# Optimization experiments

Hardware: AMD Instinct MI355X
Metric: run time of the kernel (lower is better)

## Reference

```python
import jax, jax.numpy as jnp
import numpy as np

NTOKEN, NINP, NCLASS = 50000, 256, 16
B, L = 32, 2048
INITRANGE = 0.1


def setup_inputs() -> dict:
    key = jax.random.key(0)
    k1, k2, k3 = jax.random.split(key, 3)
    inp = jax.random.randint(k1, (B, L), 0, NTOKEN).astype(jnp.int64) if jax.config.jax_enable_x64 else jax.random.randint(k1, (B, L), 0, NTOKEN)
    mask = jnp.ones((B, L), dtype=jnp.float32)
    enc_w = jax.random.uniform(k2, (NTOKEN + 1, NINP), jnp.float32, -INITRANGE, INITRANGE)
    dec_w = jax.random.uniform(k3, (NCLASS, NINP), jnp.float32, -INITRANGE, INITRANGE)
    return {"input": inp, "mask": mask, "enc_w": enc_w, "dec_w": dec_w}


def reference(input, mask, enc_w, dec_w):
    # emb: [B, L, D], masked embedding gather
    emb = enc_w[input] * mask[:, :, None]
    # scores_l = emb_l . sum_k emb_k  ==  (emb @ emb^T).sum(axis=2)
    emb_sum = emb.sum(axis=1)                         # [B, D]
    scores = jnp.einsum('bld,bd->bl', emb, emb_sum)   # [B, L]
    y = jnp.exp(scores) * mask                        # faithful: no max-subtract
    attn = y / y.sum(axis=1, keepdims=True)           # [B, L]
    output = jnp.einsum('bld,bl->bd', emb, attn)      # weighted-sum pooling
    # residual mean pooling
    lens = mask.sum(axis=1, keepdims=True)            # [B, 1]
    avg = emb_sum / lens
    out = output + avg
    return out @ dec_w.T                              # [B, NCLASS]
```

## Files before the change

kernel.cpp:

```cpp
#include <hip/hip_runtime.h>
#include <math.h>

#define BB 32
#define LL 2048
#define DD 256
#define NC 16
#define SPLIT 32
#define TPB 256
#define TOK_PER_CHUNK (LL / SPLIT)
#define TOK_PER_WAVE  (TOK_PER_CHUNK / 4)
#define PF 8


__global__ __launch_bounds__(TPB) void kA_partial(
    const int* __restrict__ idx, const float* __restrict__ mask,
    const float4* __restrict__ enc4,
    float* __restrict__ pes, float* __restrict__ plen) {
  const int b     = blockIdx.x / SPLIT;
  const int chunk = blockIdx.x % SPLIT;
  const int wave  = threadIdx.x >> 6;
  const int lane  = threadIdx.x & 63;
  const int tid   = threadIdx.x;
  const int l0 = chunk * TOK_PER_CHUNK + wave * TOK_PER_WAVE;

  int   id_r[TOK_PER_WAVE];
  float m_r[TOK_PER_WAVE];
  #pragma unroll
  for (int t = 0; t < TOK_PER_WAVE; ++t) {
    id_r[t] = idx[b * LL + l0 + t];
    m_r[t]  = mask[b * LL + l0 + t];
  }

  float4 acc = {0.f, 0.f, 0.f, 0.f};
  float lenacc = 0.f;
  #pragma unroll
  for (int g = 0; g < TOK_PER_WAVE; g += PF) {
    float4 v[PF];
    #pragma unroll
    for (int t = 0; t < PF; ++t)
      v[t] = enc4[(size_t)id_r[g + t] * (DD / 4) + lane];
    #pragma unroll
    for (int t = 0; t < PF; ++t) {
      const float m = m_r[g + t];
      acc.x += v[t].x * m; acc.y += v[t].y * m;
      acc.z += v[t].z * m; acc.w += v[t].w * m;
      lenacc += m;
    }
  }

  __shared__ float lds[4][DD];
  __shared__ float llds[4];
  lds[wave][lane * 4 + 0] = acc.x;
  lds[wave][lane * 4 + 1] = acc.y;
  lds[wave][lane * 4 + 2] = acc.z;
  lds[wave][lane * 4 + 3] = acc.w;
  if (lane == 0) llds[wave] = lenacc;
  __syncthreads();

  const float s = lds[0][tid] + lds[1][tid] + lds[2][tid] + lds[3][tid];
  pes[(chunk * BB + b) * DD + tid] = s;
  if (tid == 0) plen[chunk * BB + b] = llds[0] + llds[1] + llds[2] + llds[3];
}

__global__ __launch_bounds__(TPB) void kR1(
    const float* __restrict__ pes, const float* __restrict__ plen,
    float* __restrict__ emb_sum, float* __restrict__ lens) {
  const int b = blockIdx.x;
  const int tid = threadIdx.x;
  float s = 0.f;
  #pragma unroll
  for (int c = 0; c < SPLIT; ++c) s += pes[(c * BB + b) * DD + tid];
  emb_sum[b * DD + tid] = s;
  if (tid < 64) {
    float v = (tid < SPLIT) ? plen[tid * BB + b] : 0.f;
    #pragma unroll
    for (int off = 16; off > 0; off >>= 1) v += __shfl_xor(v, off);
    if (tid == 0) lens[b] = v;
  }
}

__global__ __launch_bounds__(TPB) void kB_partial(
    const int* __restrict__ idx, const float* __restrict__ mask,
    const float4* __restrict__ enc4, const float* __restrict__ emb_sum,
    float* __restrict__ pout, float* __restrict__ pys) {
  const int b     = blockIdx.x / SPLIT;
  const int chunk = blockIdx.x % SPLIT;
  const int wave  = threadIdx.x >> 6;
  const int lane  = threadIdx.x & 63;
  const int tid   = threadIdx.x;
  const int l0 = chunk * TOK_PER_CHUNK + wave * TOK_PER_WAVE;

  const float4 es = reinterpret_cast<const float4*>(emb_sum)[b * (DD / 4) + lane];

  int   id_r[TOK_PER_WAVE];
  float m_r[TOK_PER_WAVE];
  #pragma unroll
  for (int t = 0; t < TOK_PER_WAVE; ++t) {
    id_r[t] = idx[b * LL + l0 + t];
    m_r[t]  = mask[b * LL + l0 + t];
  }

  float4 acc = {0.f, 0.f, 0.f, 0.f};
  float ys = 0.f;
  #pragma unroll
  for (int g = 0; g < TOK_PER_WAVE; g += PF) {
    float4 v[PF];
    #pragma unroll
    for (int t = 0; t < PF; ++t)
      v[t] = enc4[(size_t)id_r[g + t] * (DD / 4) + lane];
    #pragma unroll
    for (int t = 0; t < PF; ++t) {
      const float m = m_r[g + t];
      float d = v[t].x * es.x + v[t].y * es.y + v[t].z * es.z + v[t].w * es.w;
      #pragma unroll
      for (int off = 32; off > 0; off >>= 1) d += __shfl_xor(d, off);
      const float score = d * m;
      const float y = expf(score) * m;
      const float ym = y * m;
      acc.x += ym * v[t].x; acc.y += ym * v[t].y;
      acc.z += ym * v[t].z; acc.w += ym * v[t].w;
      ys += y;
    }
  }

  __shared__ float lds[4][DD];
  __shared__ float ylds[4];
  lds[wave][lane * 4 + 0] = acc.x;
  lds[wave][lane * 4 + 1] = acc.y;
  lds[wave][lane * 4 + 2] = acc.z;
  lds[wave][lane * 4 + 3] = acc.w;
  if (lane == 0) ylds[wave] = ys;
  __syncthreads();

  const float s = lds[0][tid] + lds[1][tid] + lds[2][tid] + lds[3][tid];
  pout[(chunk * BB + b) * DD + tid] = s;
  if (tid == 0) pys[chunk * BB + b] = ylds[0] + ylds[1] + ylds[2] + ylds[3];
}

__global__ __launch_bounds__(TPB) void kR2head(
    const float* __restrict__ pout, const float* __restrict__ pys,
    const float* __restrict__ emb_sum, const float* __restrict__ lens,
    const float* __restrict__ dec_w, float* __restrict__ out) {
  const int b = blockIdx.x;
  const int tid = threadIdx.x;
  const int wave = tid >> 6;
  const int lane = tid & 63;

  float os = 0.f;
  #pragma unroll
  for (int c = 0; c < SPLIT; ++c) os += pout[(c * BB + b) * DD + tid];

  __shared__ float ysum_s;
  __shared__ float vec[DD];
  if (tid < 64) {
    float v = (tid < SPLIT) ? pys[tid * BB + b] : 0.f;
    #pragma unroll
    for (int off = 16; off > 0; off >>= 1) v += __shfl_xor(v, off);
    if (tid == 0) ysum_s = v;
  }
  __syncthreads();

  vec[tid] = os / ysum_s + emb_sum[b * DD + tid] / lens[b];
  __syncthreads();

  const float4 vv = *reinterpret_cast<const float4*>(&vec[lane * 4]);
  #pragma unroll
  for (int cc = 0; cc < 4; ++cc) {
    const int c = wave * 4 + cc;
    const float4 dw = reinterpret_cast<const float4*>(dec_w)[c * (DD / 4) + lane];
    float d = vv.x * dw.x + vv.y * dw.y + vv.z * dw.z + vv.w * dw.w;
    #pragma unroll
    for (int off = 32; off > 0; off >>= 1) d += __shfl_xor(d, off);
    if (lane == 0) out[b * NC + c] = d;
  }
}

extern "C" void kernel_launch(void* const* d_in, const int* in_sizes, int n_in,
                              void* d_out, int out_size, void* d_ws, size_t ws_size,
                              hipStream_t stream) {
  const int*   idx   = (const int*)d_in[0];
  const float* mask  = (const float*)d_in[1];
  const float* enc_w = (const float*)d_in[2];
  const float* dec_w = (const float*)d_in[3];
  float* out = (float*)d_out;

  float* ws = (float*)d_ws;
  float* pes     = ws;
  float* plen    = pes + SPLIT * BB * DD;
  float* pout    = plen + SPLIT * BB;
  float* pys     = pout + SPLIT * BB * DD;
  float* emb_sum = pys + SPLIT * BB;
  float* lens    = emb_sum + BB * DD;

  const dim3 block(TPB);
  const dim3 gridP(BB * SPLIT);
  hipLaunchKernelGGL(kA_partial, gridP, block, 0, stream,
                     idx, mask, (const float4*)enc_w, pes, plen);
  hipLaunchKernelGGL(kR1, dim3(BB), block, 0, stream, pes, plen, emb_sum, lens);
  hipLaunchKernelGGL(kB_partial, gridP, block, 0, stream,
                     idx, mask, (const float4*)enc_w, emb_sum, pout, pys);
  hipLaunchKernelGGL(kR2head, dim3(BB), block, 0, stream,
                     pout, pys, emb_sum, lens, dec_w, out);
}
```

Before: 33.12 us.

## Fuse first reduction into second pass and rebalance split counts

Removes the separate kR1 reduction kernel. Each block of the second pass now reduces the per-chunk partial embedding sums itself into shared memory, and chunk 0 writes emb_sum and lens. The second pass split drops from 32 to 16 chunks, giving more tokens per wave, and the first pass now issues all 16 gathers up front instead of in groups of 8. This saves one kernel launch and its dependency gap, but every block of the second pass re-reads the 32 partials, and the deeper register arrays can raise register pressure.

```diff
diff --git a/kernel.cpp b/kernel.cpp
--- a/kernel.cpp
+++ b/kernel.cpp
@@ -5,47 +5,49 @@
 #define LL 2048
 #define DD 256
 #define NC 16
-#define SPLIT 32
 #define TPB 256
-#define TOK_PER_CHUNK (LL / SPLIT)
-#define TOK_PER_WAVE  (TOK_PER_CHUNK / 4)
-#define PF 8
+
+#define SA 32
+#define TA_CHUNK (LL / SA)
+#define TA_WAVE  (TA_CHUNK / 4)
+
+#define SB 16
+#define TB_CHUNK (LL / SB)
+#define TB_WAVE  (TB_CHUNK / 4)
+#define PFB 8
 
 
 __global__ __launch_bounds__(TPB) void kA_partial(
     const int* __restrict__ idx, const float* __restrict__ mask,
     const float4* __restrict__ enc4,
     float* __restrict__ pes, float* __restrict__ plen) {
-  const int b     = blockIdx.x / SPLIT;
-  const int chunk = blockIdx.x % SPLIT;
+  const int b     = blockIdx.x / SA;
+  const int chunk = blockIdx.x % SA;
   const int wave  = threadIdx.x >> 6;
   const int lane  = threadIdx.x & 63;
   const int tid   = threadIdx.x;
-  const int l0 = chunk * TOK_PER_CHUNK + wave * TOK_PER_WAVE;
-
-  int   id_r[TOK_PER_WAVE];
-  float m_r[TOK_PER_WAVE];
-  #pragma unroll
-  for (int t = 0; t < TOK_PER_WAVE; ++t) {
+  const int l0 = chunk * TA_CHUNK + wave * TA_WAVE;
+
+  int   id_r[TA_WAVE];
+  float m_r[TA_WAVE];
+  #pragma unroll
+  for (int t = 0; t < TA_WAVE; ++t) {
     id_r[t] = idx[b * LL + l0 + t];
     m_r[t]  = mask[b * LL + l0 + t];
   }
+  float4 v_r[TA_WAVE];
+  #pragma unroll
+  for (int t = 0; t < TA_WAVE; ++t)
+    v_r[t] = enc4[(size_t)id_r[t] * (DD / 4) + lane];
 
   float4 acc = {0.f, 0.f, 0.f, 0.f};
   float lenacc = 0.f;
   #pragma unroll
-  for (int g = 0; g < TOK_PER_WAVE; g += PF) {
-    float4 v[PF];
-    #pragma unroll
-    for (int t = 0; t < PF; ++t)
-      v[t] = enc4[(size_t)id_r[g + t] * (DD / 4) + lane];
-    #pragma unroll
-    for (int t = 0; t < PF; ++t) {
-      const float m = m_r[g + t];
-      acc.x += v[t].x * m; acc.y += v[t].y * m;
-      acc.z += v[t].z * m; acc.w += v[t].w * m;
-      lenacc += m;
-    }
+  for (int t = 0; t < TA_WAVE; ++t) {
+    const float m = m_r[t];
+    acc.x += v_r[t].x * m; acc.y += v_r[t].y * m;
+    acc.z += v_r[t].z * m; acc.w += v_r[t].w * m;
+    lenacc += m;
   }
 
   __shared__ float lds[4][DD];
@@ -62,40 +64,45 @@
   if (tid == 0) plen[chunk * BB + b] = llds[0] + llds[1] + llds[2] + llds[3];
 }
 
-__global__ __launch_bounds__(TPB) void kR1(
+__global__ __launch_bounds__(TPB) void kB_fused(
+    const int* __restrict__ idx, const float* __restrict__ mask,
+    const float4* __restrict__ enc4,
     const float* __restrict__ pes, const float* __restrict__ plen,
+    float* __restrict__ pout, float* __restrict__ pys,
     float* __restrict__ emb_sum, float* __restrict__ lens) {
-  const int b = blockIdx.x;
-  const int tid = threadIdx.x;
-  float s = 0.f;
-  #pragma unroll
-  for (int c = 0; c < SPLIT; ++c) s += pes[(c * BB + b) * DD + tid];
-  emb_sum[b * DD + tid] = s;
-  if (tid < 64) {
-    float v = (tid < SPLIT) ? plen[tid * BB + b] : 0.f;
-    #pragma unroll
-    for (int off = 16; off > 0; off >>= 1) v += __shfl_xor(v, off);
-    if (tid == 0) lens[b] = v;
-  }
-}
-
-__global__ __launch_bounds__(TPB) void kB_partial(
-    const int* __restrict__ idx, const float* __restrict__ mask,
-    const float4* __restrict__ enc4, const float* __restrict__ emb_sum,
-    float* __restrict__ pout, float* __restrict__ pys) {
-  const int b     = blockIdx.x / SPLIT;
-  const int chunk = blockIdx.x % SPLIT;
+  const int b     = blockIdx.x / SB;
+  const int chunk = blockIdx.x % SB;
   const int wave  = threadIdx.x >> 6;
   const int lane  = threadIdx.x & 63;
   const int tid   = threadIdx.x;
-  const int l0 = chunk * TOK_PER_CHUNK + wave * TOK_PER_WAVE;
-
-  const float4 es = reinterpret_cast<const float4*>(emb_sum)[b * (DD / 4) + lane];
-
-  int   id_r[TOK_PER_WAVE];
-  float m_r[TOK_PER_WAVE];
-  #pragma unroll
-  for (int t = 0; t < TOK_PER_WAVE; ++t) {
+  const int l0 = chunk * TB_CHUNK + wave * TB_WAVE;
+
+  __shared__ __align__(16) float esb[DD];
+  __shared__ float lds[4][DD];
+  __shared__ float ylds[4];
+
+  {
+    float es_col = 0.f;
+    #pragma unroll
+    for (int c = 0; c < SA; ++c) es_col += pes[(c * BB + b) * DD + tid];
+    esb[tid] = es_col;
+    if (chunk == 0) {
+      emb_sum[b * DD + tid] = es_col;
+      if (tid < 64) {
+        float v = (tid < SA) ? plen[tid * BB + b] : 0.f;
+        #pragma unroll
+        for (int off = 16; off > 0; off >>= 1) v += __shfl_xor(v, off);
+        if (tid == 0) lens[b] = v;
+      }
+    }
+  }
+  __syncthreads();
+  const float4 es = *reinterpret_cast<const float4*>(&esb[lane * 4]);
+
+  int   id_r[TB_WAVE];
+  float m_r[TB_WAVE];
+  #pragma unroll
+  for (int t = 0; t < TB_WAVE; ++t) {
     id_r[t] = idx[b * LL + l0 + t];
     m_r[t]  = mask[b * LL + l0 + t];
   }
@@ -103,13 +110,13 @@
   float4 acc = {0.f, 0.f, 0.f, 0.f};
   float ys = 0.f;
   #pragma unroll
-  for (int g = 0; g < TOK_PER_WAVE; g += PF) {
-    float4 v[PF];
-    #pragma unroll
-    for (int t = 0; t < PF; ++t)
+  for (int g = 0; g < TB_WAVE; g += PFB) {
+    float4 v[PFB];
+    #pragma unroll
+    for (int t = 0; t < PFB; ++t)
       v[t] = enc4[(size_t)id_r[g + t] * (DD / 4) + lane];
     #pragma unroll
-    for (int t = 0; t < PF; ++t) {
+    for (int t = 0; t < PFB; ++t) {
       const float m = m_r[g + t];
       float d = v[t].x * es.x + v[t].y * es.y + v[t].z * es.z + v[t].w * es.w;
       #pragma unroll
@@ -123,8 +130,6 @@
     }
   }
 
-  __shared__ float lds[4][DD];
-  __shared__ float ylds[4];
   lds[wave][lane * 4 + 0] = acc.x;
   lds[wave][lane * 4 + 1] = acc.y;
   lds[wave][lane * 4 + 2] = acc.z;
@@ -148,12 +153,12 @@
 
   float os = 0.f;
   #pragma unroll
-  for (int c = 0; c < SPLIT; ++c) os += pout[(c * BB + b) * DD + tid];
+  for (int c = 0; c < SB; ++c) os += pout[(c * BB + b) * DD + tid];
 
   __shared__ float ysum_s;
-  __shared__ float vec[DD];
+  __shared__ __align__(16) float vec[DD];
   if (tid < 64) {
-    float v = (tid < SPLIT) ? pys[tid * BB + b] : 0.f;
+    float v = (tid < SB) ? pys[tid * BB + b] : 0.f;
     #pragma unroll
     for (int off = 16; off > 0; off >>= 1) v += __shfl_xor(v, off);
     if (tid == 0) ysum_s = v;
@@ -178,27 +183,25 @@
 extern "C" void kernel_launch(void* const* d_in, const int* in_sizes, int n_in,
                               void* d_out, int out_size, void* d_ws, size_t ws_size,
                               hipStream_t stream) {
-  const int*   idx   = (const int*)d_in[0];
-  const float* mask  = (const float*)d_in[1];
-  const float* enc_w = (const float*)d_in[2];
-  const float* dec_w = (const float*)d_in[3];
+  const int*    idx   = (const int*)d_in[0];
+  const float*  mask  = (const float*)d_in[1];
+  const float4* enc4  = (const float4*)d_in[2];
+  const float*  dec_w = (const float*)d_in[3];
   float* out = (float*)d_out;
 
   float* ws = (float*)d_ws;
   float* pes     = ws;
-  float* plen    = pes + SPLIT * BB * DD;
-  float* pout    = plen + SPLIT * BB;
-  float* pys     = pout + SPLIT * BB * DD;
-  float* emb_sum = pys + SPLIT * BB;
+  float* plen    = pes + SA * BB * DD;
+  float* pout    = plen + SA * BB;
+  float* pys     = pout + SB * BB * DD;
+  float* emb_sum = pys + SB * BB;
   float* lens    = emb_sum + BB * DD;
 
   const dim3 block(TPB);
-  const dim3 gridP(BB * SPLIT);
-  hipLaunchKernelGGL(kA_partial, gridP, block, 0, stream,
-                     idx, mask, (const float4*)enc_w, pes, plen);
-  hipLaunchKernelGGL(kR1, dim3(BB), block, 0, stream, pes, plen, emb_sum, lens);
-  hipLaunchKernelGGL(kB_partial, gridP, block, 0, stream,
-                     idx, mask, (const float4*)enc_w, emb_sum, pout, pys);
+  hipLaunchKernelGGL(kA_partial, dim3(BB * SA), block, 0, stream,
+                     idx, mask, enc4, pes, plen);
+  hipLaunchKernelGGL(kB_fused, dim3(BB * SB), block, 0, stream,
+                     idx, mask, enc4, pes, plen, pout, pys, emb_sum, lens);
   hipLaunchKernelGGL(kR2head, dim3(BB), block, 0, stream,
                      pout, pys, emb_sum, lens, dec_w, out);
 }
```

After: 36.16 us. 9.2% more time.
